# Kernel optimization log

Measured on AMD Instinct MI355X. Metric: run time of the kernel, lower is better.

## Reference

```python
import jax, jax.numpy as jnp
import numpy as np
from jax import lax

A = 3          # anchors per scale
C = 80         # num foreground classes (COCO)
NMS_THRESH = 0.45
NMS_TOPK = 400
POST_NMS = 100


def setup_inputs() -> dict:
    key = jax.random.key(0)
    k0, k1, k2 = jax.random.split(key, 3)
    B = 8
    ch = A * (C + 5)  # 255
    # raw head outputs (pre-decode conv activations), modest scale so exp() stays sane
    tip0 = jax.random.normal(k0, (B, ch, 19, 19), jnp.float32) * 0.5
    tip1 = jax.random.normal(k1, (B, ch, 38, 38), jnp.float32) * 0.5
    tip2 = jax.random.normal(k2, (B, ch, 76, 76), jnp.float32) * 0.5
    # standard YOLOv3 COCO anchors, deepest scale (stride 32) first
    anchors0 = jnp.array([[116., 90.], [156., 198.], [373., 326.]], jnp.float32)
    anchors1 = jnp.array([[30., 61.], [62., 45.], [59., 119.]], jnp.float32)
    anchors2 = jnp.array([[10., 13.], [16., 30.], [33., 23.]], jnp.float32)
    return dict(tip0=tip0, tip1=tip1, tip2=tip2,
                anchors0=anchors0, anchors1=anchors1, anchors2=anchors2)


def _decode(tip, anchors, stride):
    """YOLOOutputV3 inference decode. tip: (B, A*(C+5), H, W)."""
    B, _, H, W = tip.shape
    # (B, A*(C+5), H*W) -> (B, H*W, A, C+5)
    pred = tip.reshape(B, A * (C + 5), H * W).transpose(0, 2, 1).reshape(B, H * W, A, C + 5)
    gx, gy = jnp.meshgrid(jnp.arange(W), jnp.arange(H))       # each (H, W)
    offsets = jnp.stack([gx, gy], -1).reshape(1, H * W, 1, 2).astype(tip.dtype)
    centers = (jax.nn.sigmoid(pred[..., :2]) + offsets) * stride          # (B,HW,A,2)
    scales = jnp.exp(pred[..., 2:4]) * anchors.reshape(1, 1, A, 2)        # (B,HW,A,2)
    conf = jax.nn.sigmoid(pred[..., 4:5])                                 # objectness
    cls_scores = jax.nn.sigmoid(pred[..., 5:]) * conf                      # (B,HW,A,C)
    wh = scales * 0.5
    bbox = jnp.concatenate([centers - wh, centers + wh], -1)               # corner format
    return bbox.reshape(B, H * W * A, 4), cls_scores.reshape(B, H * W * A, C)


def _pairwise_iou(b):
    """b: (K,4) corner boxes -> (K,K) IoU."""
    x1, y1, x2, y2 = b[:, 0], b[:, 1], b[:, 2], b[:, 3]
    area = jnp.maximum(x2 - x1, 0.) * jnp.maximum(y2 - y1, 0.)
    iw = jnp.maximum(jnp.minimum(x2[:, None], x2[None, :]) - jnp.maximum(x1[:, None], x1[None, :]), 0.)
    ih = jnp.maximum(jnp.minimum(y2[:, None], y2[None, :]) - jnp.maximum(y1[:, None], y1[None, :]), 0.)
    inter = iw * ih
    return inter / (area[:, None] + area[None, :] - inter + 1e-12)


def _nms_single(det):
    """Class-aware greedy NMS on one image. det: (M,6) = (cid, score, x1,y1,x2,y2)."""
    K = NMS_TOPK
    _, idx = lax.top_k(det[:, 1], K)     # sort by score, keep top K
    d = det[idx]                          # (K,6), descending score
    iou = _pairwise_iou(d[:, 2:6])
    same = d[:, 0][:, None] == d[:, 0][None, :]   # only same class suppresses
    valid = d[:, 1] > 0.
    rng = jnp.arange(K)

    def body(i, keep):
        sup = (iou[i] > NMS_THRESH) & same[i] & (rng > i) & keep[i] & valid[i]
        return keep & ~sup

    keep = lax.fori_loop(0, K, body, jnp.ones((K,), bool)) & valid
    d = jnp.where(keep[:, None], d, jnp.full_like(d, -1.))
    order = jnp.argsort(-d[:, 1])         # kept (sorted) first, suppressed (-1) last
    return d[order][:POST_NMS]            # (POST_NMS, 6)


def _detect(tip0, tip1, tip2, anchors0, anchors1, anchors2):
    dets = []
    for tip, anc, stride in ((tip0, anchors0, 32), (tip1, anchors1, 16), (tip2, anchors2, 8)):
        bbox, scores = _decode(tip, anc, stride)          # (B,N,4), (B,N,C)
        B, N, _ = bbox.shape
        ids = jnp.broadcast_to(jnp.arange(C, dtype=bbox.dtype)[None, None, :, None], (B, N, C, 1))
        sc = scores[..., None]                            # (B,N,C,1)
        bx = jnp.broadcast_to(bbox[:, :, None, :], (B, N, C, 4))
        dets.append(jnp.concatenate([ids, sc, bx], -1).reshape(B, N * C, 6))
    det = jnp.concatenate(dets, 1)                        # (B, M, 6)
    return jax.vmap(_nms_single)(det)                     # (B, POST_NMS, 6)


def reference(tip0, tip1, tip2, anchors0, anchors1, anchors2):
    res = _detect(tip0, tip1, tip2, anchors0, anchors1, anchors2)
    ids = res[..., 0:1]
    scores = res[..., 1:2]
    bboxes = res[..., 2:6]
    return ids, scores, bboxes
```

## Files before the change

### kernel.cpp

```cpp
#include <hip/hip_runtime.h>
#include <stdint.h>

#define NUMA 3
#define NUMC 80
#define CAP  49152
#define KTOP 400
#define POST 100
#define EQCAP 1024
#define PFCAP 2048
#define KEY0 0x3EE66666u
#define KEYTOP 0x3F800000u
#define LBUF 1024
#define NMASK (KTOP * 7)

typedef float f32x4 __attribute__((ext_vector_type(4)));

__device__ __forceinline__ float sigmoidf_(float x) { return 1.0f / (1.0f + expf(-x)); }
__device__ __forceinline__ unsigned uminu(unsigned a, unsigned b) { return a < b ? a : b; }

__device__ __forceinline__ float thr_for(float cf) {
    if (!(cf >= 0.45f)) return 3.0e38f;
    float q = 0.449f / cf;
    float r = q / (1.0f - q);
    return logf(r) - 0.01f;
}

__global__ void init_kernel(unsigned* __restrict__ p) {
    int i = blockIdx.x * blockDim.x + threadIdx.x;
    if (i < 24) p[i] = 0;
}

__global__ __launch_bounds__(256) void score_main(
        const float* __restrict__ t0, const float* __restrict__ t1,
        const float* __restrict__ t2,
        unsigned* __restrict__ ccnt, unsigned* __restrict__ ckey,
        unsigned* __restrict__ cidx)
{
    __shared__ unsigned lkey[LBUF], lidx[LBUF];
    __shared__ unsigned lcnt, lbase;
    const int tid = threadIdx.x;
    if (tid == 0) lcnt = 0;
    __syncthreads();

    const int ba = blockIdx.z;
    const int b = ba / 3, a = ba - 3 * b;
    const int c0 = blockIdx.y * 10;
    const int cx = blockIdx.x;

    #define LEMIT(SC, IDX) do { \
        unsigned key_ = __float_as_uint(SC); \
        if (key_ >= KEY0) { \
            unsigned pos_ = atomicAdd(&lcnt, 1u); \
            if (pos_ < LBUF) { lkey[pos_] = key_; lidx[pos_] = (IDX); } \
        } \
    } while (0)

    if (cx < 2) {
        const int hw = cx * 256 + tid;
        if (hw < 361) {
            const float* base = t0 + (size_t)(b * 255 + a * 85) * 361;
            float cr = base[4 * 361 + hw];
            const float* p0 = base + (size_t)(5 + c0) * 361 + hw;
            float x0 = p0[0 * 361], x1 = p0[1 * 361], x2 = p0[2 * 361], x3 = p0[3 * 361];
            float x4 = p0[4 * 361], x5 = p0[5 * 361], x6 = p0[6 * 361], x7 = p0[7 * 361];
            float x8 = p0[8 * 361], x9 = p0[9 * 361];
            float cf = sigmoidf_(cr);
            float xt = thr_for(cf);
            unsigned ib = (unsigned)((hw * NUMA + a) * NUMC + c0);
            if (x0 > xt) LEMIT(sigmoidf_(x0) * cf, ib + 0);
            if (x1 > xt) LEMIT(sigmoidf_(x1) * cf, ib + 1);
            if (x2 > xt) LEMIT(sigmoidf_(x2) * cf, ib + 2);
            if (x3 > xt) LEMIT(sigmoidf_(x3) * cf, ib + 3);
            if (x4 > xt) LEMIT(sigmoidf_(x4) * cf, ib + 4);
            if (x5 > xt) LEMIT(sigmoidf_(x5) * cf, ib + 5);
            if (x6 > xt) LEMIT(sigmoidf_(x6) * cf, ib + 6);
            if (x7 > xt) LEMIT(sigmoidf_(x7) * cf, ib + 7);
            if (x8 > xt) LEMIT(sigmoidf_(x8) * cf, ib + 8);
            if (x9 > xt) LEMIT(sigmoidf_(x9) * cf, ib + 9);
        }
    } else {
        const float* tip; int vHW, v, candOff;
        if (cx < 4) { tip = t1; vHW = 361;  v = (cx - 2) * 256 + tid; candOff = 86640; }
        else        { tip = t2; vHW = 1444; v = (cx - 4) * 256 + tid; candOff = 433200; }
        if (v < vHW) {
            const f32x4* bp = (const f32x4*)(tip + (size_t)(b * 255 + a * 85) * (size_t)(vHW * 4));
            f32x4 cv = bp[(size_t)4 * vHW + v];
            const f32x4* p0 = bp + (size_t)(5 + c0) * vHW + v;
            f32x4 s0 = p0[0 * (size_t)vHW], s1 = p0[1 * (size_t)vHW];
            f32x4 s2 = p0[2 * (size_t)vHW], s3 = p0[3 * (size_t)vHW];
            f32x4 s4 = p0[4 * (size_t)vHW], s5 = p0[5 * (size_t)vHW];
            f32x4 s6 = p0[6 * (size_t)vHW], s7 = p0[7 * (size_t)vHW];
            f32x4 s8 = p0[8 * (size_t)vHW], s9 = p0[9 * (size_t)vHW];
            float cf0 = sigmoidf_(cv[0]), cf1 = sigmoidf_(cv[1]);
            float cf2 = sigmoidf_(cv[2]), cf3 = sigmoidf_(cv[3]);
            float xt0 = thr_for(cf0), xt1 = thr_for(cf1);
            float xt2 = thr_for(cf2), xt3 = thr_for(cf3);
            unsigned ib0 = (unsigned)(candOff + (v * 4 * NUMA + a) * NUMC + c0);
            #define EMIT4(S, U) do { \
                unsigned ib = ib0 + (U); \
                if ((S)[0] > xt0) LEMIT(sigmoidf_((S)[0]) * cf0, ib); \
                if ((S)[1] > xt1) LEMIT(sigmoidf_((S)[1]) * cf1, ib + 240); \
                if ((S)[2] > xt2) LEMIT(sigmoidf_((S)[2]) * cf2, ib + 480); \
                if ((S)[3] > xt3) LEMIT(sigmoidf_((S)[3]) * cf3, ib + 720); \
            } while (0)
            EMIT4(s0, 0); EMIT4(s1, 1); EMIT4(s2, 2); EMIT4(s3, 3);
            EMIT4(s4, 4); EMIT4(s5, 5); EMIT4(s6, 6); EMIT4(s7, 7);
            EMIT4(s8, 8); EMIT4(s9, 9);
            #undef EMIT4
        }
    }
    #undef LEMIT

    __syncthreads();
    if (tid == 0) {
        unsigned c = lcnt;
        if (c > LBUF) {
            atomicOr(&ccnt[b], 0x80000000u);
            lbase = 0xFFFFFFFFu;
        } else {
            lbase = atomicAdd(&ccnt[b], c);
        }
    }
    __syncthreads();
    unsigned c = uminu(lcnt, (unsigned)LBUF);
    unsigned basep = lbase;
    if (basep != 0xFFFFFFFFu) {
        for (unsigned i = tid; i < c; i += 256) {
            unsigned p = basep + i;
            if (p < CAP) {
                ckey[(size_t)b * CAP + p] = lkey[i];
                cidx[(size_t)b * CAP + p] = lidx[i];
            }
        }
    }
}

__device__ __forceinline__ void wave_select(const unsigned* h, int nbins, unsigned rank,
                                            unsigned* resv, int tid)
{
    if (tid >= 64) return;
    const int lane = tid;
    const int cs = nbins >> 6;
    unsigned v = 0;
    for (int k = 0; k < cs; k++) {
        int off = (k + lane) & (cs - 1);
        v += h[lane * cs + off];
    }
    unsigned S = v;
    #pragma unroll
    for (int o = 1; o < 64; o <<= 1) {
        unsigned t = (unsigned)__shfl_down((int)S, o);
        if (lane + o < 64) S += t;
    }
    unsigned long long bm = __ballot(S >= rank);
    if (bm == 0ull) bm = 1ull;
    int C = 63 - __builtin_clzll(bm);
    unsigned SC = (unsigned)__builtin_amdgcn_readlane((int)S, C);
    unsigned vC = (unsigned)__builtin_amdgcn_readlane((int)v, C);
    unsigned rem = rank - (SC - vC);
    unsigned w = (lane < cs) ? h[C * cs + lane] : 0u;
    unsigned T = w;
    #pragma unroll
    for (int o = 1; o < 64; o <<= 1) {
        unsigned t = (unsigned)__shfl_down((int)T, o);
        if (lane + o < 64) T += t;
    }
    unsigned long long bm2 = __ballot((T >= rem) && (lane < cs));
    if (bm2 == 0ull) bm2 = 1ull;
    int B = 63 - __builtin_clzll(bm2);
    unsigned TB = (unsigned)__builtin_amdgcn_readlane((int)T, B);
    unsigned wB = (unsigned)__builtin_amdgcn_readlane((int)w, B);
    if (lane == 0) {
        resv[0] = (unsigned)(C * cs + B);
        resv[1] = rem - (TB - wB);
    }
}

__global__ __launch_bounds__(1024) void fb_all(
        const float* __restrict__ t0, const float* __restrict__ t1,
        const float* __restrict__ t2,
        unsigned* __restrict__ cutb, unsigned* __restrict__ ccnt,
        unsigned* __restrict__ flags,
        unsigned* __restrict__ ckey, unsigned* __restrict__ cidx)
{
    const int b = blockIdx.x;
    unsigned cc = ccnt[b];
    if (cc >= KTOP && cc <= CAP) return;

    __shared__ unsigned lh[2048];
    __shared__ unsigned resv[2];
    __shared__ unsigned fcnt;
    const int tid = threadIdx.x;
    const int NPOS = 3 * (361 + 1444 + 5776);

    for (int i = tid; i < 2048; i += 1024) lh[i] = 0;
    if (tid == 0) fcnt = 0;
    __syncthreads();

    for (int p = tid; p < NPOS; p += 1024) {
        const float* tip; int HW, pp;
        if (p < 1083)      { tip = t0; HW = 361;  pp = p; }
        else if (p < 5415) { tip = t1; HW = 1444; pp = p - 1083; }
        else               { tip = t2; HW = 5776; pp = p - 5415; }
        int a = pp / HW, hwl = pp - a * HW;
        const float* base = tip + (size_t)(b * 255 + a * 85) * HW;
        float cf = sigmoidf_(base[4 * HW + hwl]);
        for (int u = 0; u < NUMC; u++) {
            float sc = sigmoidf_(base[(size_t)(5 + u) * HW + hwl]) * cf;
            atomicAdd(&lh[__float_as_uint(sc) >> 19], 1u);
        }
    }
    __syncthreads();
    wave_select(lh, 2048, KTOP, resv, tid);
    __syncthreads();
    unsigned cutbin = resv[0];
    unsigned cutkey = cutbin << 19;
    __syncthreads();

    unsigned* ck = ckey + (size_t)b * CAP;
    unsigned* ci = cidx + (size_t)b * CAP;
    for (int p = tid; p < NPOS; p += 1024) {
        const float* tip; int HW, pp, candOff;
        if (p < 1083)      { tip = t0; HW = 361;  pp = p;        candOff = 0; }
        else if (p < 5415) { tip = t1; HW = 1444; pp = p - 1083; candOff = 86640; }
        else               { tip = t2; HW = 5776; pp = p - 5415; candOff = 433200; }
        int a = pp / HW, hwl = pp - a * HW;
        const float* base = tip + (size_t)(b * 255 + a * 85) * HW;
        float cf = sigmoidf_(base[4 * HW + hwl]);
        unsigned ib0 = (unsigned)(candOff + (hwl * NUMA + a) * NUMC);
        for (int u = 0; u < NUMC; u++) {
            float sc = sigmoidf_(base[(size_t)(5 + u) * HW + hwl]) * cf;
            unsigned key = __float_as_uint(sc);
            if (key >= cutkey) {
                unsigned pos = atomicAdd(&fcnt, 1u);
                if (pos < CAP) { ck[pos] = key; ci[pos] = ib0 + (unsigned)u; }
            }
        }
    }
    __syncthreads();
    if (tid == 0) { ccnt[b] = fcnt; cutb[b] = cutbin; flags[b] = 1u; }
}

__global__ __launch_bounds__(1024) void topk_sel(
        const float* __restrict__ t0, const float* __restrict__ t1,
        const float* __restrict__ t2,
        const float* __restrict__ anc0, const float* __restrict__ anc1,
        const float* __restrict__ anc2,
        const unsigned* __restrict__ ckey, const unsigned* __restrict__ cidx,
        const unsigned* __restrict__ ccnt, const unsigned* __restrict__ cutb,
        const unsigned* __restrict__ flags,
        float* __restrict__ dX1, float* __restrict__ dY1,
        float* __restrict__ dX2, float* __restrict__ dY2,
        float* __restrict__ dSC, unsigned* __restrict__ dCID)
{
    const int b = blockIdx.x;
    const int tid = threadIdx.x;
    const int T = 1024;

    __shared__ unsigned hist[4096];
    __shared__ unsigned resv[2];
    __shared__ unsigned selk[512], seli[512];
    __shared__ unsigned eqi[EQCAP];
    __shared__ unsigned pk[PFCAP], pi[PFCAP];
    __shared__ unsigned cnts[3];

    const unsigned* ck = ckey + (size_t)b * CAP;
    const unsigned* ci = cidx + (size_t)b * CAP;
    unsigned n = uminu(ccnt[b], (unsigned)CAP);

    unsigned kbase = flags[b] ? (cutb[b] << 19) : KEY0;
    unsigned span = (KEYTOP - kbase) + 1u;
    unsigned SH = 0;
    while ((span >> SH) > 2047u) SH++;

    for (int i = tid; i < 2048; i += T) hist[i] = 0;
    __syncthreads();
    {
        unsigned n4 = n >> 2;
        const uint4* ck4 = (const uint4*)ck;
        for (unsigned i = tid; i < n4; i += T) {
            uint4 k = ck4[i];
            atomicAdd(&hist[(k.x - kbase) >> SH], 1u);
            atomicAdd(&hist[(k.y - kbase) >> SH], 1u);
            atomicAdd(&hist[(k.z - kbase) >> SH], 1u);
            atomicAdd(&hist[(k.w - kbase) >> SH], 1u);
        }
        for (unsigned i = (n4 << 2) + tid; i < n; i += T)
            atomicAdd(&hist[(ck[i] - kbase) >> SH], 1u);
    }
    __syncthreads();
    wave_select(hist, 2048, KTOP, resv, tid);
    __syncthreads();
    unsigned Bf = resv[0];
    __syncthreads();

    if (tid == 0) { cnts[0] = 0; cnts[1] = 0; cnts[2] = 0; }
    __syncthreads();
    for (unsigned i = tid; i < n; i += T) {
        unsigned k = ck[i];
        if (((k - kbase) >> SH) >= Bf) {
            unsigned q = atomicAdd(&cnts[2], 1u);
            if (q < (unsigned)PFCAP) { pk[q] = k; pi[q] = ci[i]; }
        }
    }
    __syncthreads();
    unsigned pfCnt = cnts[2];
    bool useP = (pfCnt <= (unsigned)PFCAP);
    unsigned m = useP ? pfCnt : n;

    for (int i = tid; i < 4096; i += T) hist[i] = 0;
    __syncthreads();
    for (unsigned i = tid; i < m; i += T) {
        unsigned k = useP ? pk[i] : ck[i];
        atomicAdd(&hist[k >> 19], 1u);
    }
    __syncthreads();
    wave_select(hist, 4096, KTOP, resv, tid);
    __syncthreads();
    unsigned b1 = resv[0], r2 = resv[1];
    __syncthreads();

    for (int i = tid; i < 4096; i += T) hist[i] = 0;
    __syncthreads();
    for (unsigned i = tid; i < m; i += T) {
        unsigned k = useP ? pk[i] : ck[i];
        if ((k >> 19) == b1) atomicAdd(&hist[(k >> 7) & 0xFFFu], 1u);
    }
    __syncthreads();
    wave_select(hist, 4096, r2, resv, tid);
    __syncthreads();
    unsigned b2 = resv[0], r3 = resv[1];
    __syncthreads();

    for (int i = tid; i < 128; i += T) hist[i] = 0;
    __syncthreads();
    unsigned pref = (b1 << 12) | b2;
    for (unsigned i = tid; i < m; i += T) {
        unsigned k = useP ? pk[i] : ck[i];
        if ((k >> 7) == pref) atomicAdd(&hist[k & 127u], 1u);
    }
    __syncthreads();
    wave_select(hist, 128, r3, resv, tid);
    __syncthreads();
    unsigned b3 = resv[0], needEq = resv[1];
    unsigned K400 = (b1 << 19) | (b2 << 7) | b3;
    __syncthreads();

    for (int i = tid; i < 512; i += T) { selk[i] = 0u; seli[i] = 0xFFFFFFFFu; }
    for (int i = tid; i < EQCAP; i += T) eqi[i] = 0xFFFFFFFFu;
    __syncthreads();
    for (unsigned i = tid; i < m; i += T) {
        unsigned k = useP ? pk[i] : ck[i];
        if (k > K400) {
            unsigned idx = useP ? pi[i] : ci[i];
            unsigned p = atomicAdd(&cnts[0], 1u);
            if (p < 512u) { selk[p] = k; seli[p] = idx; }
        } else if (k == K400) {
            unsigned idx = useP ? pi[i] : ci[i];
            unsigned q = atomicAdd(&cnts[1], 1u);
            if (q < (unsigned)EQCAP) eqi[q] = idx;
        }
    }
    __syncthreads();
    unsigned selCnt = uminu(cnts[0], (unsigned)KTOP);
    unsigned eqN   = uminu(cnts[1], (unsigned)EQCAP);

    if (eqN > needEq) {
        int P2 = 1; while ((unsigned)P2 < eqN) P2 <<= 1;
        for (int k2 = 2; k2 <= P2; k2 <<= 1) {
            for (int j = k2 >> 1; j > 0; j >>= 1) {
                __syncthreads();
                for (int i = tid; i < P2; i += T) {
                    int ixj = i ^ j;
                    if (ixj > i && ixj < P2) {
                        unsigned va = eqi[i], vb = eqi[ixj];
                        bool up = ((i & k2) == 0);
                        if (up ? (va > vb) : (va < vb)) { eqi[i] = vb; eqi[ixj] = va; }
                    }
                }
            }
        }
        __syncthreads();
    }
    for (unsigned t2v = tid; t2v < needEq; t2v += T) {
        unsigned p = selCnt + t2v;
        if (p < KTOP) { selk[p] = K400; seli[p] = eqi[t2v]; }
    }
    __syncthreads();

    for (int k2 = 2; k2 <= 512; k2 <<= 1) {
        int j = k2 >> 1;
        for (; j >= 64; j >>= 1) {
            __syncthreads();
            if (tid < 512) {
                int i = tid, ixj = i ^ j;
                if (ixj > i) {
                    unsigned ka = selk[i], kb = selk[ixj], ia = seli[i], ib = seli[ixj];
                    bool before = (ka > kb) || (ka == kb && ia < ib);
                    bool up = ((i & k2) == 0);
                    if (up ? !before : before) {
                        selk[i] = kb; selk[ixj] = ka; seli[i] = ib; seli[ixj] = ia;
                    }
                }
            }
        }
        __syncthreads();
        if (tid < 512) {
            for (; j > 0; j >>= 1) {
                int i = tid, ixj = i ^ j;
                if (ixj > i) {
                    unsigned ka = selk[i], kb = selk[ixj], ia = seli[i], ib = seli[ixj];
                    bool before = (ka > kb) || (ka == kb && ia < ib);
                    bool up = ((i & k2) == 0);
                    if (up ? !before : before) {
                        selk[i] = kb; selk[ixj] = ka; seli[i] = ib; seli[ixj] = ia;
                    }
                }
            }
        }
    }
    __syncthreads();

    if (tid < KTOP) {
        unsigned idx = seli[tid];
        int o = b * KTOP + tid;
        if (idx == 0xFFFFFFFFu) {
            dX1[o] = -1.f; dY1[o] = -1.f; dX2[o] = -1.f; dY2[o] = -1.f;
            dSC[o] = __uint_as_float(selk[tid]); dCID[o] = 0u;
        } else {
            const float* tip; const float* anc; int HW, W, candOff; float strideF;
            if (idx < 86640u)       { tip = t0; anc = anc0; HW = 361;  W = 19; strideF = 32.f; candOff = 0; }
            else if (idx < 433200u) { tip = t1; anc = anc1; HW = 1444; W = 38; strideF = 16.f; candOff = 86640; }
            else                    { tip = t2; anc = anc2; HW = 5776; W = 76; strideF = 8.f;  candOff = 433200; }
            unsigned local = idx - (unsigned)candOff;
            int cls = (int)(local % NUMC);
            int nn  = (int)(local / NUMC);
            int a = nn % NUMA, hwl = nn / NUMA;
            const float* base = tip + (size_t)(b * 255 + a * 85) * HW + hwl;
            float tx = base[0];
            float ty = base[(size_t)HW];
            float tw = base[(size_t)2 * HW];
            float th = base[(size_t)3 * HW];
            float fx = (float)(hwl % W), fy = (float)(hwl / W);
            float cx = (sigmoidf_(tx) + fx) * strideF;
            float cy = (sigmoidf_(ty) + fy) * strideF;
            float hw_ = expf(tw) * anc[2 * a]     * 0.5f;
            float hh_ = expf(th) * anc[2 * a + 1] * 0.5f;
            dX1[o] = cx - hw_; dY1[o] = cy - hh_;
            dX2[o] = cx + hw_; dY2[o] = cy + hh_;
            dSC[o] = __uint_as_float(selk[tid]);
            dCID[o] = (unsigned)cls;
        }
    }
}

__global__ __launch_bounds__(256) void mask_kernel(
        const float* __restrict__ dX1, const float* __restrict__ dY1,
        const float* __restrict__ dX2, const float* __restrict__ dY2,
        const unsigned* __restrict__ dCID, unsigned long long* __restrict__ maskG)
{
    __shared__ float lx1[KTOP], ly1[KTOP], lx2[KTOP], ly2[KTOP];
    __shared__ int lcid[KTOP];
    const int b = blockIdx.y;
    const int tid = threadIdx.x;
    for (int i = tid; i < KTOP; i += 256) {
        int o = b * KTOP + i;
        lx1[i] = dX1[o]; ly1[i] = dY1[o];
        lx2[i] = dX2[o]; ly2[i] = dY2[o];
        lcid[i] = (int)dCID[o];
    }
    __syncthreads();
    int p = blockIdx.x * 256 + tid;
    if (p < NMASK) {
        int i = p / 7, w = p - i * 7;
        float x1i = lx1[i], y1i = ly1[i], x2i = lx2[i], y2i = ly2[i];
        float ai = fmaxf(x2i - x1i, 0.f) * fmaxf(y2i - y1i, 0.f);
        int cidI = lcid[i];
        unsigned long long m = 0ull;
        int j0 = w * 64;
        int rot = (9 * w) & 63;
        for (int t = 0; t < 64; t++) {
            int j = j0 + ((t + rot) & 63);
            if (j >= KTOP || j <= i) continue;
            if (lcid[j] != cidI) continue;
            float iw = fminf(x2i, lx2[j]) - fmaxf(x1i, lx1[j]);
            float ih = fminf(y2i, ly2[j]) - fmaxf(y1i, ly1[j]);
            iw = fmaxf(iw, 0.f); ih = fmaxf(ih, 0.f);
            float inter = iw * ih;
            float aj = fmaxf(lx2[j] - lx1[j], 0.f) * fmaxf(ly2[j] - ly1[j], 0.f);
            float iou = inter / (ai + aj - inter + 1e-12f);
            if (iou > 0.45f) m |= (1ull << (j - j0));
        }
        maskG[(size_t)b * NMASK + p] = m;
    }
}

__global__ __launch_bounds__(512) void greedy_kernel(
        const float* __restrict__ dX1, const float* __restrict__ dY1,
        const float* __restrict__ dX2, const float* __restrict__ dY2,
        const float* __restrict__ dSC, const unsigned* __restrict__ dCID,
        const unsigned long long* __restrict__ maskG, float* __restrict__ out)
{
    __shared__ unsigned long long maskL[NMASK];
    __shared__ unsigned long long vkeep[7];
    __shared__ float oid[POST], osc[POST], obb[POST * 4];
    const int b = blockIdx.x;
    const int tid = threadIdx.x;

    for (int i = tid; i < NMASK; i += 512) maskL[i] = maskG[(size_t)b * NMASK + i];
    if (tid < POST) { oid[tid] = -1.f; osc[tid] = -1.f; }
    if (tid < POST * 4) obb[tid] = -1.f;
    __syncthreads();

    if (tid < 64) {
        const int lane = tid;
        unsigned long long keep = 0ull;
        if (lane < 7) keep = (lane == 6) ? 0xFFFFull : ~0ull;
        unsigned long long mb[8];
        #pragma unroll
        for (int k = 0; k < 8; k++)
            mb[k] = (lane < 7) ? maskL[k * 7 + lane] : 0ull;
        for (int ib = 0; ib < KTOP; ib += 8) {
            #pragma unroll
            for (int k = 0; k < 8; k++) {
                int i = ib + k;
                unsigned long long m = mb[k];
                int nf = ib + 8 + k;
                mb[k] = (lane < 7 && nf < KTOP) ? maskL[nf * 7 + lane] : 0ull;
                int w = i >> 6;
                unsigned klo = (unsigned)__builtin_amdgcn_readlane((int)(unsigned)(keep & 0xFFFFFFFFull), w);
                unsigned khi = (unsigned)__builtin_amdgcn_readlane((int)(unsigned)(keep >> 32), w);
                unsigned long long kw = ((unsigned long long)khi << 32) | klo;
                if ((kw >> (i & 63)) & 1ull) keep &= ~m;
            }
        }
        if (lane < 7) vkeep[lane] = keep;
    }
    __syncthreads();

    if (tid < KTOP) {
        int w = tid >> 6, bp = tid & 63;
        unsigned long long kw = vkeep[w];
        if ((kw >> bp) & 1ull) {
            int r = 0;
            for (int q = 0; q < w; q++) r += __popcll(vkeep[q]);
            r += __popcll(kw & ((1ull << bp) - 1ull));
            if (r < POST) {
                int o = b * KTOP + tid;
                oid[r] = (float)(int)dCID[o];
                osc[r] = dSC[o];
                obb[r * 4 + 0] = dX1[o];
                obb[r * 4 + 1] = dY1[o];
                obb[r * 4 + 2] = dX2[o];
                obb[r * 4 + 3] = dY2[o];
            }
        }
    }
    __syncthreads();
    if (tid < POST) {
        out[b * POST + tid]       = oid[tid];
        out[800 + b * POST + tid] = osc[tid];
    }
    if (tid < POST * 4) out[1600 + b * POST * 4 + tid] = obb[tid];
}

extern "C" void kernel_launch(void* const* d_in, const int* in_sizes, int n_in,
                              void* d_out, int out_size, void* d_ws, size_t ws_size,
                              hipStream_t stream)
{
    const float* tip0 = (const float*)d_in[0];
    const float* tip1 = (const float*)d_in[1];
    const float* tip2 = (const float*)d_in[2];
    const float* anc0 = (const float*)d_in[3];
    const float* anc1 = (const float*)d_in[4];
    const float* anc2 = (const float*)d_in[5];
    float* out = (float*)d_out;

    unsigned* cutb  = (unsigned*)d_ws;
    unsigned* ccnt  = cutb + 8;
    unsigned* flags = ccnt + 8;
    unsigned* ckey  = flags + 8;
    unsigned* cidx  = ckey + (size_t)8 * CAP;
    float*    dX1   = (float*)(cidx + (size_t)8 * CAP);
    float*    dY1   = dX1 + 8 * KTOP;
    float*    dX2   = dY1 + 8 * KTOP;
    float*    dY2   = dX2 + 8 * KTOP;
    float*    dSC   = dY2 + 8 * KTOP;
    unsigned* dCID  = (unsigned*)(dSC + 8 * KTOP);
    unsigned long long* maskG = (unsigned long long*)(dCID + 8 * KTOP);

    init_kernel<<<1, 64, 0, stream>>>(cutb);

    dim3 g(10, 8, 24);
    score_main<<<g, 256, 0, stream>>>(tip0, tip1, tip2, ccnt, ckey, cidx);
    fb_all<<<8, 1024, 0, stream>>>(tip0, tip1, tip2, cutb, ccnt, flags, ckey, cidx);
    topk_sel<<<8, 1024, 0, stream>>>(tip0, tip1, tip2, anc0, anc1, anc2,
                                     ckey, cidx, ccnt, cutb, flags,
                                     dX1, dY1, dX2, dY2, dSC, dCID);
    mask_kernel<<<dim3((NMASK + 255) / 256, 8), 256, 0, stream>>>(
        dX1, dY1, dX2, dY2, dCID, maskG);
    greedy_kernel<<<8, 512, 0, stream>>>(dX1, dY1, dX2, dY2, dSC, dCID, maskG, out);
}
```

Before: 191.3 us.

## Fold fallback path into topk_sel and fuse IoU mask with greedy NMS

Removes the separate fb_all kernel by running its rare fallback (full-histogram cut and re-collect) inside topk_sel when the candidate count is out of range. It also merges mask_kernel and greedy_kernel into one nms_kernel that builds the suppression mask in shared memory, then runs the greedy scan and writes output from shared copies. This saves two launches and the global round-trip of the mask. The cost is that the IoU mask is now built by only 8 blocks instead of a wider grid.

```diff
diff --git a/kernel.cpp b/kernel.cpp
--- a/kernel.cpp
+++ b/kernel.cpp
@@ -27,7 +27,7 @@
 
 __global__ void init_kernel(unsigned* __restrict__ p) {
     int i = blockIdx.x * blockDim.x + threadIdx.x;
-    if (i < 24) p[i] = 0;
+    if (i < 8) p[i] = 0;
 }
 
 __global__ __launch_bounds__(256) void score_main(
@@ -176,79 +176,13 @@
     }
 }
 
-__global__ __launch_bounds__(1024) void fb_all(
-        const float* __restrict__ t0, const float* __restrict__ t1,
-        const float* __restrict__ t2,
-        unsigned* __restrict__ cutb, unsigned* __restrict__ ccnt,
-        unsigned* __restrict__ flags,
-        unsigned* __restrict__ ckey, unsigned* __restrict__ cidx)
-{
-    const int b = blockIdx.x;
-    unsigned cc = ccnt[b];
-    if (cc >= KTOP && cc <= CAP) return;
-
-    __shared__ unsigned lh[2048];
-    __shared__ unsigned resv[2];
-    __shared__ unsigned fcnt;
-    const int tid = threadIdx.x;
-    const int NPOS = 3 * (361 + 1444 + 5776);
-
-    for (int i = tid; i < 2048; i += 1024) lh[i] = 0;
-    if (tid == 0) fcnt = 0;
-    __syncthreads();
-
-    for (int p = tid; p < NPOS; p += 1024) {
-        const float* tip; int HW, pp;
-        if (p < 1083)      { tip = t0; HW = 361;  pp = p; }
-        else if (p < 5415) { tip = t1; HW = 1444; pp = p - 1083; }
-        else               { tip = t2; HW = 5776; pp = p - 5415; }
-        int a = pp / HW, hwl = pp - a * HW;
-        const float* base = tip + (size_t)(b * 255 + a * 85) * HW;
-        float cf = sigmoidf_(base[4 * HW + hwl]);
-        for (int u = 0; u < NUMC; u++) {
-            float sc = sigmoidf_(base[(size_t)(5 + u) * HW + hwl]) * cf;
-            atomicAdd(&lh[__float_as_uint(sc) >> 19], 1u);
-        }
-    }
-    __syncthreads();
-    wave_select(lh, 2048, KTOP, resv, tid);
-    __syncthreads();
-    unsigned cutbin = resv[0];
-    unsigned cutkey = cutbin << 19;
-    __syncthreads();
-
-    unsigned* ck = ckey + (size_t)b * CAP;
-    unsigned* ci = cidx + (size_t)b * CAP;
-    for (int p = tid; p < NPOS; p += 1024) {
-        const float* tip; int HW, pp, candOff;
-        if (p < 1083)      { tip = t0; HW = 361;  pp = p;        candOff = 0; }
-        else if (p < 5415) { tip = t1; HW = 1444; pp = p - 1083; candOff = 86640; }
-        else               { tip = t2; HW = 5776; pp = p - 5415; candOff = 433200; }
-        int a = pp / HW, hwl = pp - a * HW;
-        const float* base = tip + (size_t)(b * 255 + a * 85) * HW;
-        float cf = sigmoidf_(base[4 * HW + hwl]);
-        unsigned ib0 = (unsigned)(candOff + (hwl * NUMA + a) * NUMC);
-        for (int u = 0; u < NUMC; u++) {
-            float sc = sigmoidf_(base[(size_t)(5 + u) * HW + hwl]) * cf;
-            unsigned key = __float_as_uint(sc);
-            if (key >= cutkey) {
-                unsigned pos = atomicAdd(&fcnt, 1u);
-                if (pos < CAP) { ck[pos] = key; ci[pos] = ib0 + (unsigned)u; }
-            }
-        }
-    }
-    __syncthreads();
-    if (tid == 0) { ccnt[b] = fcnt; cutb[b] = cutbin; flags[b] = 1u; }
-}
-
 __global__ __launch_bounds__(1024) void topk_sel(
         const float* __restrict__ t0, const float* __restrict__ t1,
         const float* __restrict__ t2,
         const float* __restrict__ anc0, const float* __restrict__ anc1,
         const float* __restrict__ anc2,
-        const unsigned* __restrict__ ckey, const unsigned* __restrict__ cidx,
-        const unsigned* __restrict__ ccnt, const unsigned* __restrict__ cutb,
-        const unsigned* __restrict__ flags,
+        const unsigned* __restrict__ ccnt,
+        unsigned* __restrict__ ckey, unsigned* __restrict__ cidx,
         float* __restrict__ dX1, float* __restrict__ dY1,
         float* __restrict__ dX2, float* __restrict__ dY2,
         float* __restrict__ dSC, unsigned* __restrict__ dCID)
@@ -263,12 +197,60 @@
     __shared__ unsigned eqi[EQCAP];
     __shared__ unsigned pk[PFCAP], pi[PFCAP];
     __shared__ unsigned cnts[3];
-
-    const unsigned* ck = ckey + (size_t)b * CAP;
-    const unsigned* ci = cidx + (size_t)b * CAP;
-    unsigned n = uminu(ccnt[b], (unsigned)CAP);
-
-    unsigned kbase = flags[b] ? (cutb[b] << 19) : KEY0;
+    __shared__ unsigned fcnt;
+
+    unsigned* ck = ckey + (size_t)b * CAP;
+    unsigned* ci = cidx + (size_t)b * CAP;
+    unsigned nraw = ccnt[b];
+    unsigned kbase = KEY0;
+
+    if (!(nraw >= KTOP && nraw <= CAP)) {
+        const int NPOS = 3 * (361 + 1444 + 5776);
+        for (int i = tid; i < 2048; i += T) hist[i] = 0;
+        if (tid == 0) fcnt = 0;
+        __syncthreads();
+        for (int p = tid; p < NPOS; p += T) {
+            const float* tip; int HW, pp;
+            if (p < 1083)      { tip = t0; HW = 361;  pp = p; }
+            else if (p < 5415) { tip = t1; HW = 1444; pp = p - 1083; }
+            else               { tip = t2; HW = 5776; pp = p - 5415; }
+            int a = pp / HW, hwl = pp - a * HW;
+            const float* base = tip + (size_t)(b * 255 + a * 85) * HW;
+            float cf = sigmoidf_(base[4 * HW + hwl]);
+            for (int u = 0; u < NUMC; u++) {
+                float sc = sigmoidf_(base[(size_t)(5 + u) * HW + hwl]) * cf;
+                atomicAdd(&hist[__float_as_uint(sc) >> 19], 1u);
+            }
+        }
+        __syncthreads();
+        wave_select(hist, 2048, KTOP, resv, tid);
+        __syncthreads();
+        unsigned cutkey = resv[0] << 19;
+        __syncthreads();
+        for (int p = tid; p < NPOS; p += T) {
+            const float* tip; int HW, pp, candOff;
+            if (p < 1083)      { tip = t0; HW = 361;  pp = p;        candOff = 0; }
+            else if (p < 5415) { tip = t1; HW = 1444; pp = p - 1083; candOff = 86640; }
+            else               { tip = t2; HW = 5776; pp = p - 5415; candOff = 433200; }
+            int a = pp / HW, hwl = pp - a * HW;
+            const float* base = tip + (size_t)(b * 255 + a * 85) * HW;
+            float cf = sigmoidf_(base[4 * HW + hwl]);
+            unsigned ib0 = (unsigned)(candOff + (hwl * NUMA + a) * NUMC);
+            for (int u = 0; u < NUMC; u++) {
+                float sc = sigmoidf_(base[(size_t)(5 + u) * HW + hwl]) * cf;
+                unsigned key = __float_as_uint(sc);
+                if (key >= cutkey) {
+                    unsigned pos = atomicAdd(&fcnt, 1u);
+                    if (pos < CAP) { ck[pos] = key; ci[pos] = ib0 + (unsigned)u; }
+                }
+            }
+        }
+        __syncthreads();
+        nraw = fcnt;
+        kbase = cutkey;
+    }
+    unsigned n = uminu(nraw, (unsigned)CAP);
+
     unsigned span = (KEYTOP - kbase) + 1u;
     unsigned SH = 0;
     while ((span >> SH) > 2047u) SH++;
@@ -454,24 +436,29 @@
     }
 }
 
-__global__ __launch_bounds__(256) void mask_kernel(
+__global__ __launch_bounds__(1024) void nms_kernel(
         const float* __restrict__ dX1, const float* __restrict__ dY1,
         const float* __restrict__ dX2, const float* __restrict__ dY2,
-        const unsigned* __restrict__ dCID, unsigned long long* __restrict__ maskG)
+        const float* __restrict__ dSC, const unsigned* __restrict__ dCID,
+        float* __restrict__ out)
 {
-    __shared__ float lx1[KTOP], ly1[KTOP], lx2[KTOP], ly2[KTOP];
+    __shared__ float lx1[KTOP], ly1[KTOP], lx2[KTOP], ly2[KTOP], lsc[KTOP];
     __shared__ int lcid[KTOP];
-    const int b = blockIdx.y;
+    __shared__ unsigned long long maskL[NMASK];
+    __shared__ unsigned long long vkeep[7];
+    __shared__ float oid[POST], osc[POST], obb[POST * 4];
+    const int b = blockIdx.x;
     const int tid = threadIdx.x;
-    for (int i = tid; i < KTOP; i += 256) {
+
+    for (int i = tid; i < KTOP; i += 1024) {
         int o = b * KTOP + i;
         lx1[i] = dX1[o]; ly1[i] = dY1[o];
         lx2[i] = dX2[o]; ly2[i] = dY2[o];
-        lcid[i] = (int)dCID[o];
-    }
-    __syncthreads();
-    int p = blockIdx.x * 256 + tid;
-    if (p < NMASK) {
+        lsc[i] = dSC[o]; lcid[i] = (int)dCID[o];
+    }
+    __syncthreads();
+
+    for (int p = tid; p < NMASK; p += 1024) {
         int i = p / 7, w = p - i * 7;
         float x1i = lx1[i], y1i = ly1[i], x2i = lx2[i], y2i = ly2[i];
         float ai = fmaxf(x2i - x1i, 0.f) * fmaxf(y2i - y1i, 0.f);
@@ -491,25 +478,8 @@
             float iou = inter / (ai + aj - inter + 1e-12f);
             if (iou > 0.45f) m |= (1ull << (j - j0));
         }
-        maskG[(size_t)b * NMASK + p] = m;
-    }
-}
-
-__global__ __launch_bounds__(512) void greedy_kernel(
-        const float* __restrict__ dX1, const float* __restrict__ dY1,
-        const float* __restrict__ dX2, const float* __restrict__ dY2,
-        const float* __restrict__ dSC, const unsigned* __restrict__ dCID,
-        const unsigned long long* __restrict__ maskG, float* __restrict__ out)
-{
-    __shared__ unsigned long long maskL[NMASK];
-    __shared__ unsigned long long vkeep[7];
-    __shared__ float oid[POST], osc[POST], obb[POST * 4];
-    const int b = blockIdx.x;
-    const int tid = threadIdx.x;
-
-    for (int i = tid; i < NMASK; i += 512) maskL[i] = maskG[(size_t)b * NMASK + i];
-    if (tid < POST) { oid[tid] = -1.f; osc[tid] = -1.f; }
-    if (tid < POST * 4) obb[tid] = -1.f;
+        maskL[p] = m;
+    }
     __syncthreads();
 
     if (tid < 64) {
@@ -535,6 +505,10 @@
             }
         }
         if (lane < 7) vkeep[lane] = keep;
+    } else {
+        int q = tid - 64;
+        if (q < POST) { oid[q] = -1.f; osc[q] = -1.f; }
+        if (q < POST * 4) obb[q] = -1.f;
     }
     __syncthreads();
 
@@ -546,13 +520,12 @@
             for (int q = 0; q < w; q++) r += __popcll(vkeep[q]);
             r += __popcll(kw & ((1ull << bp) - 1ull));
             if (r < POST) {
-                int o = b * KTOP + tid;
-                oid[r] = (float)(int)dCID[o];
-                osc[r] = dSC[o];
-                obb[r * 4 + 0] = dX1[o];
-                obb[r * 4 + 1] = dY1[o];
-                obb[r * 4 + 2] = dX2[o];
-                obb[r * 4 + 3] = dY2[o];
+                oid[r] = (float)lcid[tid];
+                osc[r] = lsc[tid];
+                obb[r * 4 + 0] = lx1[tid];
+                obb[r * 4 + 1] = ly1[tid];
+                obb[r * 4 + 2] = lx2[tid];
+                obb[r * 4 + 3] = ly2[tid];
             }
         }
     }
@@ -576,28 +549,22 @@
     const float* anc2 = (const float*)d_in[5];
     float* out = (float*)d_out;
 
-    unsigned* cutb  = (unsigned*)d_ws;
-    unsigned* ccnt  = cutb + 8;
-    unsigned* flags = ccnt + 8;
-    unsigned* ckey  = flags + 8;
-    unsigned* cidx  = ckey + (size_t)8 * CAP;
-    float*    dX1   = (float*)(cidx + (size_t)8 * CAP);
-    float*    dY1   = dX1 + 8 * KTOP;
-    float*    dX2   = dY1 + 8 * KTOP;
-    float*    dY2   = dX2 + 8 * KTOP;
-    float*    dSC   = dY2 + 8 * KTOP;
-    unsigned* dCID  = (unsigned*)(dSC + 8 * KTOP);
-    unsigned long long* maskG = (unsigned long long*)(dCID + 8 * KTOP);
-
-    init_kernel<<<1, 64, 0, stream>>>(cutb);
+    unsigned* ccnt = (unsigned*)d_ws;
+    unsigned* ckey = ccnt + 8;
+    unsigned* cidx = ckey + (size_t)8 * CAP;
+    float*    dX1  = (float*)(cidx + (size_t)8 * CAP);
+    float*    dY1  = dX1 + 8 * KTOP;
+    float*    dX2  = dY1 + 8 * KTOP;
+    float*    dY2  = dX2 + 8 * KTOP;
+    float*    dSC  = dY2 + 8 * KTOP;
+    unsigned* dCID = (unsigned*)(dSC + 8 * KTOP);
+
+    init_kernel<<<1, 64, 0, stream>>>(ccnt);
 
     dim3 g(10, 8, 24);
     score_main<<<g, 256, 0, stream>>>(tip0, tip1, tip2, ccnt, ckey, cidx);
-    fb_all<<<8, 1024, 0, stream>>>(tip0, tip1, tip2, cutb, ccnt, flags, ckey, cidx);
     topk_sel<<<8, 1024, 0, stream>>>(tip0, tip1, tip2, anc0, anc1, anc2,
-                                     ckey, cidx, ccnt, cutb, flags,
+                                     ccnt, ckey, cidx,
                                      dX1, dY1, dX2, dY2, dSC, dCID);
-    mask_kernel<<<dim3((NMASK + 255) / 256, 8), 256, 0, stream>>>(
-        dX1, dY1, dX2, dY2, dCID, maskG);
-    greedy_kernel<<<8, 512, 0, stream>>>(dX1, dY1, dX2, dY2, dSC, dCID, maskG, out);
-}
+    nms_kernel<<<8, 1024, 0, stream>>>(dX1, dY1, dX2, dY2, dSC, dCID, out);
+}
```

Result: slower. 200.8 us (+5.0%).
